# Performance work log

Measured on AMD Instinct MI355X. Metric: run time of the kernel, lower is better.

## Reference

```python
import jax, jax.numpy as jnp
import numpy as np

C = 512
GROUPS = 32
EPS = 1e-6

def setup_inputs() -> dict:
    key = jax.random.key(0)
    ks = jax.random.split(key, 6)
    s = 1.0 / np.sqrt(C)
    return {
        "x": jax.random.normal(ks[0], (2, C, 16, 32, 32), dtype=jnp.float32),
        "gamma": jnp.ones((C,), jnp.float32),
        "beta": jnp.zeros((C,), jnp.float32),
        "q_w": jax.random.normal(ks[1], (C, C), jnp.float32) * s,
        "q_b": jnp.zeros((C,), jnp.float32),
        "k_w": jax.random.normal(ks[2], (C, C), jnp.float32) * s,
        "k_b": jnp.zeros((C,), jnp.float32),
        "v_w": jax.random.normal(ks[3], (C, C), jnp.float32) * s,
        "v_b": jnp.zeros((C,), jnp.float32),
        "proj_w": jax.random.normal(ks[4], (C, C), jnp.float32) * s,
        "proj_b": jnp.zeros((C,), jnp.float32),
    }

def _group_norm(x, gamma, beta):
    # x: [b, c, t, h, w]
    b, c, t, h, w = x.shape
    xg = x.reshape(b, GROUPS, c // GROUPS, t, h, w)
    mean = xg.mean(axis=(2, 3, 4, 5), keepdims=True)
    var = xg.var(axis=(2, 3, 4, 5), keepdims=True)
    xg = (xg - mean) * jax.lax.rsqrt(var + EPS)
    x = xg.reshape(b, c, t, h, w)
    return x * gamma[None, :, None, None, None] + beta[None, :, None, None, None]

def _pw_conv(x, w, bias):
    # 1x1x1 conv == channel GEMM. x: [b,c,t,h,w], w: [c_out, c_in]
    y = jnp.einsum('bcthw,oc->bothw', x, w)
    return y + bias[None, :, None, None, None]

def reference(x, gamma, beta, q_w, q_b, k_w, k_b, v_w, v_b, proj_w, proj_b):
    b, c, t, h, w = x.shape
    hn = _group_norm(x, gamma, beta)
    q = _pw_conv(hn, q_w, q_b)
    k = _pw_conv(hn, k_w, k_b)
    v = _pw_conv(hn, v_w, v_b)
    # [b,c,t,h,w] -> [b*t, h*w, c]
    def to_seq(a):
        return jnp.transpose(a, (0, 2, 3, 4, 1)).reshape(b * t, h * w, c)
    q, k, v = to_seq(q), to_seq(k), to_seq(v)
    scale = 1.0 / jnp.sqrt(jnp.asarray(c, x.dtype))
    attn = jnp.einsum('bqc,bkc->bqk', q, k) * scale  # [b*t, hw, hw]
    attn = jax.nn.softmax(attn, axis=-1)
    out = jnp.einsum('bqk,bkc->bqc', attn, v)
    out = out.reshape(b, t, h, w, c).transpose(0, 4, 1, 2, 3)
    return x + _pw_conv(out, proj_w, proj_b)
```

## Files before the change

### kernel.cpp

```cpp
#include <hip/hip_runtime.h>

typedef unsigned short u16;
typedef __attribute__((ext_vector_type(8))) short bf16x8;
typedef __attribute__((ext_vector_type(4))) float f32x4;

#define DEV static __device__ __forceinline__

DEV u16 f2bf(float f) {
  union { float f; unsigned u; } x; x.f = f;
  return (u16)((x.u + 0x7FFFu + ((x.u >> 16) & 1u)) >> 16);
}
DEV float bf2f(u16 h) { union { unsigned u; float f; } x; x.u = ((unsigned)h) << 16; return x.f; }

DEV void gload16(const void* g, void* l) {
  __builtin_amdgcn_global_load_lds((const __attribute__((address_space(1))) void*)g,
                                   (__attribute__((address_space(3))) void*)l, 16, 0, 0);
}

__global__ __launch_bounds__(256) void gn_stats_a(const float* __restrict__ x,
                                                  float2* __restrict__ part) {
  const int bg = blockIdx.x >> 5, slice = blockIdx.x & 31;
  const float* base = x + (long)bg * 262144 + slice * 8192;
  float s = 0.f, q = 0.f;
#pragma unroll
  for (int i = 0; i < 8; ++i) {
    float4 v = *(const float4*)(base + i * 1024 + threadIdx.x * 4);
    s += v.x + v.y + v.z + v.w;
    q += v.x * v.x + v.y * v.y + v.z * v.z + v.w * v.w;
  }
#pragma unroll
  for (int o = 32; o; o >>= 1) { s += __shfl_xor(s, o); q += __shfl_xor(q, o); }
  __shared__ float2 red[4];
  if ((threadIdx.x & 63) == 0) red[threadIdx.x >> 6] = make_float2(s, q);
  __syncthreads();
  if (threadIdx.x == 0) {
    float S = 0.f, Q = 0.f;
    for (int i = 0; i < 4; ++i) { S += red[i].x; Q += red[i].y; }
    part[blockIdx.x] = make_float2(S, Q);
  }
}

__global__ void gn_stats_b(const float2* __restrict__ part, float2* __restrict__ stats) {
  float s = 0.f, q = 0.f;
  if (threadIdx.x < 32) {
    float2 p = part[blockIdx.x * 32 + threadIdx.x];
    s = p.x; q = p.y;
  }
#pragma unroll
  for (int o = 32; o; o >>= 1) { s += __shfl_xor(s, o); q += __shfl_xor(q, o); }
  if (threadIdx.x == 0) {
    const float inv = 1.f / 262144.f;
    float mean = s * inv;
    float var = q * inv - mean * mean;
    stats[blockIdx.x] = make_float2(mean, rsqrtf(var + 1e-6f));
  }
}

__global__ __launch_bounds__(256) void gn_apply(const float* __restrict__ x,
                                                const float* __restrict__ gamma,
                                                const float* __restrict__ beta,
                                                const float2* __restrict__ stats,
                                                u16* __restrict__ hn) {
  __shared__ u16 tile[64][65];
  const int p0 = blockIdx.x * 64, c0 = blockIdx.y * 64, bt = blockIdx.z;
  const int b = bt >> 4, t = bt & 15, tid = threadIdx.x;
  const float* xb = x + (long)b * 8388608 + t * 1024;
#pragma unroll 4
  for (int r = 0; r < 16; ++r) {
    int ci = r * 4 + (tid >> 6), pi = tid & 63;
    int c = c0 + ci;
    float2 st = stats[b * 32 + (c >> 4)];
    float v = xb[(long)c * 16384 + p0 + pi];
    v = (v - st.x) * st.y * gamma[c] + beta[c];
    tile[ci][pi] = f2bf(v);
  }
  __syncthreads();
  u16* hb = hn + ((long)bt * 1024 + p0) * 512 + c0;
#pragma unroll 4
  for (int r = 0; r < 16; ++r) {
    int pi = r * 4 + (tid >> 6), ci = tid & 63;
    hb[(long)pi * 512 + ci] = tile[ci][pi];
  }
}

__global__ __launch_bounds__(256) void wconv(const float* __restrict__ w0, const float* __restrict__ w1,
                                             const float* __restrict__ w2, const float* __restrict__ w3,
                                             u16* __restrict__ dst) {
  int e = (blockIdx.x * 256 + threadIdx.x) * 4;
  const float* src = w0;
  int which = e >> 18, off = e & 262143;
  if (which == 1) src = w1; else if (which == 2) src = w2; else if (which == 3) src = w3;
  float4 v = *(const float4*)(src + off);
  ushort4 o;
  o.x = f2bf(v.x); o.y = f2bf(v.y); o.z = f2bf(v.z); o.w = f2bf(v.w);
  *(ushort4*)(dst + e) = o;
}

__global__ void bcat(const float* __restrict__ qb, const float* __restrict__ kb,
                     const float* __restrict__ vb, float* __restrict__ dst) {
  int i = blockIdx.x * 256 + threadIdx.x;
  if (i < 512) dst[i] = qb[i];
  else if (i < 1024) dst[i] = kb[i - 512];
  else if (i < 1536) dst[i] = vb[i - 1024];
}

__global__ __launch_bounds__(256) void softmax_rows_bf16(u16* __restrict__ scores) {
  const int wave = threadIdx.x >> 6, lane = threadIdx.x & 63;
  const long row = (long)blockIdx.x * 4 + wave;
  u16* srow = scores + row * 1024;
  bf16x8 a0 = *(const bf16x8*)(srow + lane * 16);
  bf16x8 a1 = *(const bf16x8*)(srow + lane * 16 + 8);
  float v[16];
#pragma unroll
  for (int j = 0; j < 8; ++j) { v[j] = bf2f((u16)a0[j]); v[8 + j] = bf2f((u16)a1[j]); }
  float m = v[0];
#pragma unroll
  for (int j = 1; j < 16; ++j) m = fmaxf(m, v[j]);
#pragma unroll
  for (int o = 32; o; o >>= 1) m = fmaxf(m, __shfl_xor(m, o));
  const float sc = 0.044194173824159216f;
  float s = 0.f, e[16];
#pragma unroll
  for (int j = 0; j < 16; ++j) { e[j] = __expf((v[j] - m) * sc); s += e[j]; }
#pragma unroll
  for (int o = 32; o; o >>= 1) s += __shfl_xor(s, o);
  const float inv = 1.f / s;
  bf16x8 o0, o1;
#pragma unroll
  for (int j = 0; j < 8; ++j) {
    o0[j] = (short)f2bf(e[j] * inv);
    o1[j] = (short)f2bf(e[8 + j] * inv);
  }
  *(bf16x8*)(srow + lane * 16) = o0;
  *(bf16x8*)(srow + lane * 16 + 8) = o1;
}

template <int EPI>
__global__ __launch_bounds__(512, 4) void gemmk(
    const u16* __restrict__ A, int lda, long sA,
    const u16* __restrict__ B, int ldb, long sB,
    u16* __restrict__ Cv, int ldc, long sC,
    const float* __restrict__ bias, int K,
    const float* __restrict__ xin, float* __restrict__ outp,
    u16* __restrict__ vT) {
  __shared__ u16 sm[3 * 12288];
  char* smc = (char*)sm;
  const int tid = threadIdx.x, wid = tid >> 6, lane = tid & 63;
  const int wm = wid >> 2, wn = wid & 3;

  int bx = blockIdx.x, by = blockIdx.y, bz = blockIdx.z;
  {
    unsigned gx = gridDim.x, gy = gridDim.y;
    unsigned total = gx * gy * gridDim.z;
    if ((total & 7u) == 0) {
      unsigned gxy = gx * gy;
      unsigned d = (blockIdx.z * gy + blockIdx.y) * gx + blockIdx.x;
      unsigned w = (d & 7u) * (total >> 3) + (d >> 3);
      bz = w / gxy; unsigned r = w - (unsigned)bz * gxy;
      bx = r / gy;  by = r - (unsigned)bx * gy;
    }
  }
  const long m0 = (long)bx * 128, n0 = (long)by * 256;
  const char* Ab = (const char*)(A + (long)bz * sA + m0 * lda);
  const char* Bb = (const char*)(B + (long)bz * sB + n0 * ldb);
  const int NT = K >> 5;
  const long lda2 = 2L * lda, ldb2 = 2L * ldb;

  const int srow = tid >> 2;
  const int cb = ((tid & 3) * 16) ^ ((srow & 3) << 4);
  const int dA = srow * 64 + (tid & 3) * 16;
  const int dB0 = 8192 + dA, dB1 = 16384 + dA;
  const char* gA  = Ab + (long)srow * lda2 + cb;
  const char* gB0 = Bb + (long)srow * ldb2 + cb;
  const char* gB1 = Bb + (long)(srow + 128) * ldb2 + cb;

  const int lrow = lane & 15, kslot = (lane >> 4) * 16;
  const int aoff = (wm * 64 + lrow) * 64 + (kslot ^ ((lrow & 3) << 4));
  const int boff = 8192 + (wn * 64 + lrow) * 64 + (kslot ^ ((lrow & 3) << 4));

  f32x4 acc[4][4] = {};

#define STG3(off) do { gload16(gA, smc + (off) + dA); \
                       gload16(gB0, smc + (off) + dB0); \
                       gload16(gB1, smc + (off) + dB1); } while (0)

  STG3(0);
  gA += 64; gB0 += 64; gB1 += 64;
  if (NT > 1) { STG3(24576); gA += 64; gB0 += 64; gB1 += 64; }
  if (NT > 1) asm volatile("s_waitcnt vmcnt(3)" ::: "memory");
  else        asm volatile("s_waitcnt vmcnt(0)" ::: "memory");
  __builtin_amdgcn_s_barrier();

  int cb_cur = 0, cb_stg = 49152;
  for (int T = 0; T < NT; ++T) {
    const bool s2 = (T + 2 < NT);
    const char* ba = smc + cb_cur;
    bf16x8 af[4], bf[4];
#pragma unroll
    for (int mi = 0; mi < 4; ++mi) af[mi] = *(const bf16x8*)(ba + aoff + mi * 1024);
#pragma unroll
    for (int ni = 0; ni < 4; ++ni) bf[ni] = *(const bf16x8*)(ba + boff + ni * 1024);
    if (s2) { STG3(cb_stg); gA += 64; gB0 += 64; gB1 += 64; }
    __builtin_amdgcn_s_setprio(1);
#pragma unroll
    for (int mi = 0; mi < 4; ++mi)
#pragma unroll
      for (int ni = 0; ni < 4; ++ni)
        acc[mi][ni] = __builtin_amdgcn_mfma_f32_16x16x32_bf16(af[mi], bf[ni], acc[mi][ni], 0, 0, 0);
    __builtin_amdgcn_s_setprio(0);
    if (s2) asm volatile("s_waitcnt vmcnt(3)" ::: "memory");
    else    asm volatile("s_waitcnt vmcnt(0)" ::: "memory");
    __builtin_amdgcn_s_barrier();
    cb_cur = (cb_cur == 49152) ? 0 : cb_cur + 24576;
    cb_stg = (cb_stg == 49152) ? 0 : cb_stg + 24576;
  }
#undef STG3

  __syncthreads();
  {
    const int lc = lane & 15, lr = (lane >> 4) * 4;
    char* wb_ = smc + wid * 8192;
#pragma unroll
    for (int ni = 0; ni < 4; ++ni) {
      float bv = 0.f;
      if (EPI == 1) bv = bias[n0 + wn * 64 + ni * 16 + lc];
#pragma unroll
      for (int mi = 0; mi < 4; ++mi)
#pragma unroll
        for (int j = 0; j < 4; ++j) {
          int rml = mi * 16 + lr + j;
          int colb = (ni * 32 + lc * 2) ^ ((rml & 7) << 4);
          *(u16*)(wb_ + rml * 128 + colb) = f2bf(acc[mi][ni][j] + bv);
        }
    }
  }
  __syncthreads();

  if (EPI == 2) {
    const int bt = (int)(m0 >> 10), p0i = (int)(m0 & 1023);
    const int b = bt >> 4, t = bt & 15;
    const int c = tid & 255, pg = tid >> 8;
    const long base = (long)b * 8388608 + (n0 + c) * 16384L + t * 1024 + p0i + pg * 64;
    const float bv = bias[n0 + c];
    const char* rb = smc + ((pg << 2) | (c >> 6)) * 8192;
    const int c2 = (c & 63) * 2;
#pragma unroll
    for (int i = 0; i < 8; ++i) {
      float vals[8];
#pragma unroll
      for (int j = 0; j < 8; ++j) {
        int rl = i * 8 + j;
        vals[j] = bf2f(*(const u16*)(rb + rl * 128 + (c2 ^ ((rl & 7) << 4))));
      }
      float4 x0 = *(const float4*)(xin + base + i * 8);
      float4 x1 = *(const float4*)(xin + base + i * 8 + 4);
      float4 o0 = make_float4(x0.x + bv + vals[0], x0.y + bv + vals[1],
                              x0.z + bv + vals[2], x0.w + bv + vals[3]);
      float4 o1 = make_float4(x1.x + bv + vals[4], x1.y + bv + vals[5],
                              x1.z + bv + vals[6], x1.w + bv + vals[7]);
      *(float4*)(outp + base + i * 8) = o0;
      *(float4*)(outp + base + i * 8 + 4) = o1;
    }
  } else if (EPI == 1 && n0 >= 1024) {
    const int bt = (int)(m0 >> 10), p0i = (int)(m0 & 1023);
    const int c = tid & 255, pg = tid >> 8;
    u16* dst = vT + (long)bt * 524288 + (n0 - 1024 + c) * 1024 + p0i + pg * 64;
    const char* rb = smc + ((pg << 2) | (c >> 6)) * 8192;
    const int c2 = (c & 63) * 2;
#pragma unroll
    for (int i = 0; i < 8; ++i) {
      u16 tmp[8];
#pragma unroll
      for (int j = 0; j < 8; ++j) {
        int rl = i * 8 + j;
        tmp[j] = *(const u16*)(rb + rl * 128 + (c2 ^ ((rl & 7) << 4)));
      }
      *(bf16x8*)(dst + i * 8) = *(bf16x8*)tmp;
    }
  } else {
    u16* C = Cv + (long)bz * sC;
    const int c8 = tid & 31, r0e = tid >> 5;
#pragma unroll
    for (int i = 0; i < 8; ++i) {
      int r = r0e + i * 16;
      int rwid = ((r >> 6) << 2) | (c8 >> 3);
      int rr = r & 63;
      bf16x8 v = *(const bf16x8*)(smc + rwid * 8192 + rr * 128 +
                                  (((c8 & 7) * 16) ^ ((rr & 7) << 4)));
      *(bf16x8*)(C + (m0 + r) * (long)ldc + n0 + c8 * 8) = v;
    }
  }
}

extern "C" void kernel_launch(void* const* d_in, const int* in_sizes, int n_in,
                              void* d_out, int out_size, void* d_ws, size_t ws_size,
                              hipStream_t stream) {
  (void)in_sizes; (void)n_in; (void)out_size;
  const float* x      = (const float*)d_in[0];
  const float* gamma  = (const float*)d_in[1];
  const float* beta   = (const float*)d_in[2];
  const float* q_w    = (const float*)d_in[3];
  const float* q_b    = (const float*)d_in[4];
  const float* k_w    = (const float*)d_in[5];
  const float* k_b    = (const float*)d_in[6];
  const float* v_w    = (const float*)d_in[7];
  const float* v_b    = (const float*)d_in[8];
  const float* proj_w = (const float*)d_in[9];
  const float* proj_b = (const float*)d_in[10];

  const size_t OFF_WB    = 0;
  const size_t OFF_BIAS  = 2097152;
  const size_t OFF_STATS = 2103296;
  const size_t OFF_PART  = 2103808;
  const size_t OFF_HN    = 2121728;
  const size_t OFF_QK    = 35676160;
  const size_t OFF_VT    = 102785024;
  const size_t OFF_SC    = 136339456;

  char* ws = (char*)d_ws;
  u16*    wb      = (u16*)(ws + OFF_WB);
  float*  qkvbias = (float*)(ws + OFF_BIAS);
  float2* stats   = (float2*)(ws + OFF_STATS);
  float2* part    = (float2*)(ws + OFF_PART);
  u16*    hn      = (u16*)(ws + OFF_HN);
  u16*    ob      = hn;
  u16*    qk      = (u16*)(ws + OFF_QK);
  u16*    vT      = (u16*)(ws + OFF_VT);
  u16*    scores  = (u16*)(ws + OFF_SC);

  const int CH = (ws_size >= OFF_SC + 32ULL * 2097152) ? 32 : 8;

  wconv<<<1024, 256, 0, stream>>>(q_w, k_w, v_w, proj_w, wb);
  bcat<<<6, 256, 0, stream>>>(q_b, k_b, v_b, qkvbias);
  gn_stats_a<<<2048, 256, 0, stream>>>(x, part);
  gn_stats_b<<<64, 64, 0, stream>>>(part, stats);
  gn_apply<<<dim3(16, 8, 32), 256, 0, stream>>>(x, gamma, beta, stats, hn);

  gemmk<1><<<dim3(256, 6, 1), 512, 0, stream>>>(
      hn, 512, 0, wb, 512, 0, qk, 1024, 0, qkvbias, 512, nullptr, nullptr, vT);

  for (int ch = 0; ch < 32 / CH; ++ch) {
    long f0 = (long)ch * CH;
    gemmk<0><<<dim3(8, 4, CH), 512, 0, stream>>>(
        qk + f0 * 1048576, 1024, 1048576,
        qk + 512 + f0 * 1048576, 1024, 1048576,
        scores, 1024, 1048576, nullptr, 512, nullptr, nullptr, nullptr);
    softmax_rows_bf16<<<CH * 256, 256, 0, stream>>>(scores);
    gemmk<0><<<dim3(8, 2, CH), 512, 0, stream>>>(
        scores, 1024, 1048576,
        vT + f0 * 524288, 1024, 524288,
        ob + f0 * 524288, 512, 524288, nullptr, 1024, nullptr, nullptr, nullptr);
  }

  gemmk<2><<<dim3(256, 2, 1), 512, 0, stream>>>(
      ob, 512, 0, wb + 786432, 512, 0, nullptr, 0, 0, proj_b, 512,
      x, (float*)d_out, nullptr);
}
```

Measured before the change: 288.1 us.

## Replace triple-buffered 128x256 GEMM with single-buffered 128x128 tile kernel

Replaces the 512-thread, 128x256-tile GEMM with a 256-thread, 128x128-tile kernel and doubles the grid in N for every GEMM launch. The three-stage LDS ring with async global-to-LDS prefetch and vmcnt waits becomes a single buffer: each K step loads, syncs, computes, then syncs again. The LDS XOR swizzle on the MFMA operand reads is dropped. The smaller LDS footprint may allow more resident blocks, but load latency is no longer hidden behind compute, and the unswizzled reads risk bank conflicts.

```diff
diff --git a/kernel.cpp b/kernel.cpp
--- a/kernel.cpp
+++ b/kernel.cpp
@@ -136,17 +136,17 @@
 }
 
 template <int EPI>
-__global__ __launch_bounds__(512, 4) void gemmk(
+__global__ __launch_bounds__(256, 3) void gemm97(
     const u16* __restrict__ A, int lda, long sA,
     const u16* __restrict__ B, int ldb, long sB,
     u16* __restrict__ Cv, int ldc, long sC,
     const float* __restrict__ bias, int K,
     const float* __restrict__ xin, float* __restrict__ outp,
     u16* __restrict__ vT) {
-  __shared__ u16 sm[3 * 12288];
+  __shared__ u16 sm[16384];
   char* smc = (char*)sm;
   const int tid = threadIdx.x, wid = tid >> 6, lane = tid & 63;
-  const int wm = wid >> 2, wn = wid & 3;
+  const int wm = wid >> 1, wn = wid & 1;
 
   int bx = blockIdx.x, by = blockIdx.y, bz = blockIdx.z;
   {
@@ -160,47 +160,36 @@
       bx = r / gy;  by = r - (unsigned)bx * gy;
     }
   }
-  const long m0 = (long)bx * 128, n0 = (long)by * 256;
+  const long m0 = (long)bx * 128, n0 = (long)by * 128;
   const char* Ab = (const char*)(A + (long)bz * sA + m0 * lda);
   const char* Bb = (const char*)(B + (long)bz * sB + n0 * ldb);
   const int NT = K >> 5;
   const long lda2 = 2L * lda, ldb2 = 2L * ldb;
 
-  const int srow = tid >> 2;
-  const int cb = ((tid & 3) * 16) ^ ((srow & 3) << 4);
-  const int dA = srow * 64 + (tid & 3) * 16;
-  const int dB0 = 8192 + dA, dB1 = 16384 + dA;
-  const char* gA  = Ab + (long)srow * lda2 + cb;
-  const char* gB0 = Bb + (long)srow * ldb2 + cb;
-  const char* gB1 = Bb + (long)(srow + 128) * ldb2 + cb;
+  const int srow = tid >> 2, sc16 = (tid & 3) * 16;
+  const int dA = srow * 64 + sc16;
+  const char* gA = Ab + (long)srow * lda2 + sc16;
+  const char* gB = Bb + (long)srow * ldb2 + sc16;
+  const long gA1 = 64 * lda2, gB1 = 64 * ldb2;
 
   const int lrow = lane & 15, kslot = (lane >> 4) * 16;
-  const int aoff = (wm * 64 + lrow) * 64 + (kslot ^ ((lrow & 3) << 4));
-  const int boff = 8192 + (wn * 64 + lrow) * 64 + (kslot ^ ((lrow & 3) << 4));
+  const int aoff = (wm * 64 + lrow) * 64 + kslot;
+  const int boff = 8192 + (wn * 64 + lrow) * 64 + kslot;
 
   f32x4 acc[4][4] = {};
 
-#define STG3(off) do { gload16(gA, smc + (off) + dA); \
-                       gload16(gB0, smc + (off) + dB0); \
-                       gload16(gB1, smc + (off) + dB1); } while (0)
-
-  STG3(0);
-  gA += 64; gB0 += 64; gB1 += 64;
-  if (NT > 1) { STG3(24576); gA += 64; gB0 += 64; gB1 += 64; }
-  if (NT > 1) asm volatile("s_waitcnt vmcnt(3)" ::: "memory");
-  else        asm volatile("s_waitcnt vmcnt(0)" ::: "memory");
-  __builtin_amdgcn_s_barrier();
-
-  int cb_cur = 0, cb_stg = 49152;
   for (int T = 0; T < NT; ++T) {
-    const bool s2 = (T + 2 < NT);
-    const char* ba = smc + cb_cur;
+    const long ko = (long)T * 64;
+    gload16(gA + ko, smc + dA);
+    gload16(gA + gA1 + ko, smc + 4096 + dA);
+    gload16(gB + ko, smc + 8192 + dA);
+    gload16(gB + gB1 + ko, smc + 12288 + dA);
+    __syncthreads();
     bf16x8 af[4], bf[4];
 #pragma unroll
-    for (int mi = 0; mi < 4; ++mi) af[mi] = *(const bf16x8*)(ba + aoff + mi * 1024);
-#pragma unroll
-    for (int ni = 0; ni < 4; ++ni) bf[ni] = *(const bf16x8*)(ba + boff + ni * 1024);
-    if (s2) { STG3(cb_stg); gA += 64; gB0 += 64; gB1 += 64; }
+    for (int mi = 0; mi < 4; ++mi) af[mi] = *(const bf16x8*)(smc + aoff + mi * 1024);
+#pragma unroll
+    for (int ni = 0; ni < 4; ++ni) bf[ni] = *(const bf16x8*)(smc + boff + ni * 1024);
     __builtin_amdgcn_s_setprio(1);
 #pragma unroll
     for (int mi = 0; mi < 4; ++mi)
@@ -208,15 +197,9 @@
       for (int ni = 0; ni < 4; ++ni)
         acc[mi][ni] = __builtin_amdgcn_mfma_f32_16x16x32_bf16(af[mi], bf[ni], acc[mi][ni], 0, 0, 0);
     __builtin_amdgcn_s_setprio(0);
-    if (s2) asm volatile("s_waitcnt vmcnt(3)" ::: "memory");
-    else    asm volatile("s_waitcnt vmcnt(0)" ::: "memory");
-    __builtin_amdgcn_s_barrier();
-    cb_cur = (cb_cur == 49152) ? 0 : cb_cur + 24576;
-    cb_stg = (cb_stg == 49152) ? 0 : cb_stg + 24576;
-  }
-#undef STG3
-
-  __syncthreads();
+    __syncthreads();
+  }
+
   {
     const int lc = lane & 15, lr = (lane >> 4) * 4;
     char* wb_ = smc + wid * 8192;
@@ -239,55 +222,57 @@
   if (EPI == 2) {
     const int bt = (int)(m0 >> 10), p0i = (int)(m0 & 1023);
     const int b = bt >> 4, t = bt & 15;
-    const int c = tid & 255, pg = tid >> 8;
-    const long base = (long)b * 8388608 + (n0 + c) * 16384L + t * 1024 + p0i + pg * 64;
-    const float bv = bias[n0 + c];
-    const char* rb = smc + ((pg << 2) | (c >> 6)) * 8192;
-    const int c2 = (c & 63) * 2;
-#pragma unroll
-    for (int i = 0; i < 8; ++i) {
+    const int cl = tid & 127, pg = tid >> 7;
+    const long base = (long)b * 8388608 + (n0 + cl) * 16384L + t * 1024 + p0i + pg * 64;
+    const float bv = bias[n0 + cl];
+    const int c2 = (cl & 63) * 2, whi = (cl >> 6);
+#pragma unroll
+    for (int e8 = 0; e8 < 8; ++e8) {
       float vals[8];
 #pragma unroll
       for (int j = 0; j < 8; ++j) {
-        int rl = i * 8 + j;
-        vals[j] = bf2f(*(const u16*)(rb + rl * 128 + (c2 ^ ((rl & 7) << 4))));
+        int rp = pg * 64 + e8 * 8 + j;
+        int w = ((rp >> 6) << 1) | whi;
+        int rr = rp & 63;
+        vals[j] = bf2f(*(const u16*)(smc + w * 8192 + rr * 128 + (c2 ^ ((rr & 7) << 4))));
       }
-      float4 x0 = *(const float4*)(xin + base + i * 8);
-      float4 x1 = *(const float4*)(xin + base + i * 8 + 4);
+      float4 x0 = *(const float4*)(xin + base + e8 * 8);
+      float4 x1 = *(const float4*)(xin + base + e8 * 8 + 4);
       float4 o0 = make_float4(x0.x + bv + vals[0], x0.y + bv + vals[1],
                               x0.z + bv + vals[2], x0.w + bv + vals[3]);
       float4 o1 = make_float4(x1.x + bv + vals[4], x1.y + bv + vals[5],
                               x1.z + bv + vals[6], x1.w + bv + vals[7]);
-      *(float4*)(outp + base + i * 8) = o0;
-      *(float4*)(outp + base + i * 8 + 4) = o1;
+      *(float4*)(outp + base + e8 * 8) = o0;
+      *(float4*)(outp + base + e8 * 8 + 4) = o1;
     }
   } else if (EPI == 1 && n0 >= 1024) {
     const int bt = (int)(m0 >> 10), p0i = (int)(m0 & 1023);
-    const int c = tid & 255, pg = tid >> 8;
-    u16* dst = vT + (long)bt * 524288 + (n0 - 1024 + c) * 1024 + p0i + pg * 64;
-    const char* rb = smc + ((pg << 2) | (c >> 6)) * 8192;
-    const int c2 = (c & 63) * 2;
-#pragma unroll
-    for (int i = 0; i < 8; ++i) {
+    const int cl = tid & 127, pg = tid >> 7;
+    u16* dst = vT + (long)bt * 524288 + (n0 - 1024 + cl) * 1024 + p0i + pg * 64;
+    const int c2 = (cl & 63) * 2, whi = (cl >> 6);
+#pragma unroll
+    for (int e8 = 0; e8 < 8; ++e8) {
       u16 tmp[8];
 #pragma unroll
       for (int j = 0; j < 8; ++j) {
-        int rl = i * 8 + j;
-        tmp[j] = *(const u16*)(rb + rl * 128 + (c2 ^ ((rl & 7) << 4)));
+        int rp = pg * 64 + e8 * 8 + j;
+        int w = ((rp >> 6) << 1) | whi;
+        int rr = rp & 63;
+        tmp[j] = *(const u16*)(smc + w * 8192 + rr * 128 + (c2 ^ ((rr & 7) << 4)));
       }
-      *(bf16x8*)(dst + i * 8) = *(bf16x8*)tmp;
+      *(bf16x8*)(dst + e8 * 8) = *(bf16x8*)tmp;
     }
   } else {
     u16* C = Cv + (long)bz * sC;
-    const int c8 = tid & 31, r0e = tid >> 5;
+    const int c16 = tid & 15, r0e = tid >> 4;
 #pragma unroll
     for (int i = 0; i < 8; ++i) {
       int r = r0e + i * 16;
-      int rwid = ((r >> 6) << 2) | (c8 >> 3);
+      int w = ((r >> 6) << 1) | (c16 >> 3);
       int rr = r & 63;
-      bf16x8 v = *(const bf16x8*)(smc + rwid * 8192 + rr * 128 +
-                                  (((c8 & 7) * 16) ^ ((rr & 7) << 4)));
-      *(bf16x8*)(C + (m0 + r) * (long)ldc + n0 + c8 * 8) = v;
+      bf16x8 v = *(const bf16x8*)(smc + w * 8192 + rr * 128 +
+                                  (((c16 & 7) * 16) ^ ((rr & 7) << 4)));
+      *(bf16x8*)(C + (m0 + r) * (long)ldc + n0 + c16 * 8) = v;
     }
   }
 }
@@ -336,23 +321,23 @@
   gn_stats_b<<<64, 64, 0, stream>>>(part, stats);
   gn_apply<<<dim3(16, 8, 32), 256, 0, stream>>>(x, gamma, beta, stats, hn);
 
-  gemmk<1><<<dim3(256, 6, 1), 512, 0, stream>>>(
+  gemm97<1><<<dim3(256, 12, 1), 256, 0, stream>>>(
       hn, 512, 0, wb, 512, 0, qk, 1024, 0, qkvbias, 512, nullptr, nullptr, vT);
 
   for (int ch = 0; ch < 32 / CH; ++ch) {
     long f0 = (long)ch * CH;
-    gemmk<0><<<dim3(8, 4, CH), 512, 0, stream>>>(
+    gemm97<0><<<dim3(8, 8, CH), 256, 0, stream>>>(
         qk + f0 * 1048576, 1024, 1048576,
         qk + 512 + f0 * 1048576, 1024, 1048576,
         scores, 1024, 1048576, nullptr, 512, nullptr, nullptr, nullptr);
     softmax_rows_bf16<<<CH * 256, 256, 0, stream>>>(scores);
-    gemmk<0><<<dim3(8, 2, CH), 512, 0, stream>>>(
+    gemm97<0><<<dim3(8, 4, CH), 256, 0, stream>>>(
         scores, 1024, 1048576,
         vT + f0 * 524288, 1024, 524288,
         ob + f0 * 524288, 512, 524288, nullptr, 1024, nullptr, nullptr, nullptr);
   }
 
-  gemmk<2><<<dim3(256, 2, 1), 512, 0, stream>>>(
+  gemm97<2><<<dim3(256, 4, 1), 256, 0, stream>>>(
       ob, 512, 0, wb + 786432, 512, 0, nullptr, 0, 0, proj_b, 512,
       x, (float*)d_out, nullptr);
 }
```

Result: slower. 312.3 us (+8.4%).
